# Performance work log

Hardware: AMD Instinct MI355X
Metric: run time of the kernel (lower is better)

## Reference

```python
import jax, jax.numpy as jnp
import numpy as np

N_NODES = 50000
N_EDGES = 800000
N_GRAPHS = 64
IN_CH = 128
GLOBAL_DIM = 256
HIDDEN = 64
HEADS = 4
N_CLASSES = 10


def setup_inputs() -> dict:
    key = jax.random.key(0)
    ks = jax.random.split(key, 32)
    lin = lambda k, fi, fo: jax.random.normal(k, (fi, fo), jnp.float32) * 0.02
    inp = {}
    inp["x"] = jax.random.normal(ks[0], (N_NODES, IN_CH), jnp.float32)
    inp["edge_index"] = jax.random.randint(ks[1], (2, N_EDGES), 0, N_NODES)
    inp["batch"] = jnp.sort(jax.random.randint(ks[2], (N_NODES,), 0, N_GRAPHS))
    inp["global_feats"] = jax.random.normal(ks[3], (N_GRAPHS, GLOBAL_DIM), jnp.float32)
    # conv1 (in=IN_CH)
    inp["c1_Wq"] = lin(ks[4], IN_CH, HEADS * HIDDEN); inp["c1_bq"] = jnp.zeros((HEADS * HIDDEN,), jnp.float32)
    inp["c1_Wk"] = lin(ks[5], IN_CH, HEADS * HIDDEN); inp["c1_bk"] = jnp.zeros((HEADS * HIDDEN,), jnp.float32)
    inp["c1_Wv"] = lin(ks[6], IN_CH, HEADS * HIDDEN); inp["c1_bv"] = jnp.zeros((HEADS * HIDDEN,), jnp.float32)
    inp["c1_Ws"] = lin(ks[7], IN_CH, HIDDEN);         inp["c1_bs"] = jnp.zeros((HIDDEN,), jnp.float32)
    # conv2 (in=HIDDEN)
    inp["c2_Wq"] = lin(ks[8], HIDDEN, HEADS * HIDDEN); inp["c2_bq"] = jnp.zeros((HEADS * HIDDEN,), jnp.float32)
    inp["c2_Wk"] = lin(ks[9], HIDDEN, HEADS * HIDDEN); inp["c2_bk"] = jnp.zeros((HEADS * HIDDEN,), jnp.float32)
    inp["c2_Wv"] = lin(ks[10], HIDDEN, HEADS * HIDDEN); inp["c2_bv"] = jnp.zeros((HEADS * HIDDEN,), jnp.float32)
    inp["c2_Ws"] = lin(ks[11], HIDDEN, HIDDEN);         inp["c2_bs"] = jnp.zeros((HIDDEN,), jnp.float32)
    # global MLP
    inp["g_W1"] = lin(ks[12], GLOBAL_DIM, HIDDEN); inp["g_b1"] = jnp.zeros((HIDDEN,), jnp.float32)
    inp["g_W2"] = lin(ks[13], HIDDEN, HIDDEN);     inp["g_b2"] = jnp.zeros((HIDDEN,), jnp.float32)
    # head
    inp["h_W1"] = lin(ks[14], 2 * HIDDEN, HIDDEN); inp["h_b1"] = jnp.zeros((HIDDEN,), jnp.float32)
    inp["h_W2"] = lin(ks[15], HIDDEN, N_CLASSES); inp["h_b2"] = jnp.zeros((N_CLASSES,), jnp.float32)
    return inp


def _tconv(x, src, dst, Wq, bq, Wk, bk, Wv, bv, Ws, bs):
    """PyG TransformerConv, heads=HEADS, concat=False (head-mean), root skip, eval-mode (no dropout)."""
    N = x.shape[0]
    q = (x @ Wq + bq).reshape(N, HEADS, HIDDEN)
    k = (x @ Wk + bk).reshape(N, HEADS, HIDDEN)
    v = (x @ Wv + bv).reshape(N, HEADS, HIDDEN)
    # per-edge attention logits  [E, H]
    s = jnp.einsum('ehd,ehd->eh', q[dst], k[src]) / jnp.sqrt(jnp.float32(HIDDEN))
    # segment softmax over incoming edges of each dst node
    m = jax.ops.segment_max(s, dst, num_segments=N)           # [N, H]
    e = jnp.exp(s - m[dst])                                    # [E, H]
    z = jax.ops.segment_sum(e, dst, num_segments=N)           # [N, H]
    alpha = e / z[dst]                                         # [E, H] (dst always has >=1 edge here)
    agg = jax.ops.segment_sum(alpha[:, :, None] * v[src], dst, num_segments=N)  # [N, H, D]
    return agg.mean(axis=1) + x @ Ws + bs


def reference(x, edge_index, batch, global_feats,
              c1_Wq, c1_bq, c1_Wk, c1_bk, c1_Wv, c1_bv, c1_Ws, c1_bs,
              c2_Wq, c2_bq, c2_Wk, c2_bk, c2_Wv, c2_bv, c2_Ws, c2_bs,
              g_W1, g_b1, g_W2, g_b2, h_W1, h_b1, h_W2, h_b2):
    src, dst = edge_index[0], edge_index[1]
    h = jax.nn.relu(_tconv(x, src, dst, c1_Wq, c1_bq, c1_Wk, c1_bk, c1_Wv, c1_bv, c1_Ws, c1_bs))
    h = jax.nn.relu(_tconv(h, src, dst, c2_Wq, c2_bq, c2_Wk, c2_bk, c2_Wv, c2_bv, c2_Ws, c2_bs))
    # global mean pool per graph
    ssum = jax.ops.segment_sum(h, batch, num_segments=N_GRAPHS)                # [G, HIDDEN]
    cnt = jax.ops.segment_sum(jnp.ones((h.shape[0],), h.dtype), batch, num_segments=N_GRAPHS)
    patch_emb = ssum / jnp.maximum(cnt, 1.0)[:, None]
    g = jax.nn.relu(global_feats @ g_W1 + g_b1)
    g = jax.nn.relu(g @ g_W2 + g_b2)
    fused = jnp.concatenate([patch_emb, g], axis=-1)
    return jax.nn.relu(fused @ h_W1 + h_b1) @ h_W2 + h_b2
```

## Files before the change

### kernel.cpp

```cpp
#include <hip/hip_runtime.h>
#include <hip/hip_bf16.h>
#include <math.h>

#define N_NODES   50000
#define N_EDGES   800000
#define N_GRAPHS  64
#define IN_CH     128
#define GLOBAL_DIM 256
#define HIDDEN    64
#define HEADS     4
#define N_CLASSES 10
#define QKV_COLS  832
#define MAXDEG    64

typedef unsigned short ushort_t;
typedef unsigned int uint_t;
typedef unsigned char uchar_t;
typedef __attribute__((ext_vector_type(8))) short short8;
typedef __attribute__((ext_vector_type(4))) float floatx4;
typedef __attribute__((ext_vector_type(2))) float floatx2;

__device__ __forceinline__ ushort_t bf16rne(float f) {
    uint_t b = __float_as_uint(f);
    b += 0x7fffu + ((b >> 16) & 1u);
    return (ushort_t)(b >> 16);
}
__device__ __forceinline__ float4 bf4_unpack(uint_t lo, uint_t hi) {
    float4 f;
    f.x = __uint_as_float(lo << 16);
    f.y = __uint_as_float(lo & 0xffff0000u);
    f.z = __uint_as_float(hi << 16);
    f.w = __uint_as_float(hi & 0xffff0000u);
    return f;
}
__device__ __forceinline__ uchar_t fp8e4m3(float f) {
    int v = __builtin_amdgcn_cvt_pk_fp8_f32(f, 0.f, 0, false);
    return (uchar_t)(v & 0xff);
}
__device__ __forceinline__ short8 pack_bf8(float4 a, float4 b) {
    union { short8 s; ushort_t u[8]; } r;
    r.u[0] = bf16rne(a.x); r.u[1] = bf16rne(a.y);
    r.u[2] = bf16rne(a.z); r.u[3] = bf16rne(a.w);
    r.u[4] = bf16rne(b.x); r.u[5] = bf16rne(b.y);
    r.u[6] = bf16rne(b.z); r.u[7] = bf16rne(b.w);
    return r.s;
}
__device__ __forceinline__ void graph_range(const int* __restrict__ batch, int g,
                                            int& start, int& end) {
    int lo = 0, hi = N_NODES;
    while (lo < hi) { int mid = (lo + hi) >> 1; if (batch[mid] < g) lo = mid + 1; else hi = mid; }
    start = lo;
    hi = N_NODES;
    while (lo < hi) { int mid = (lo + hi) >> 1; if (batch[mid] < g + 1) lo = mid + 1; else hi = mid; }
    end = lo;
}

#define PREP_CONC_B  624

__global__ __launch_bounds__(256) void prep2(
        const float* __restrict__ W1q, const float* __restrict__ W1k,
        const float* __restrict__ W1v, const float* __restrict__ W1s,
        const float* __restrict__ b1q, const float* __restrict__ b1k,
        const float* __restrict__ b1v, const float* __restrict__ b1s,
        const float* __restrict__ W2q, const float* __restrict__ W2k,
        const float* __restrict__ W2v, const float* __restrict__ W2s,
        const float* __restrict__ b2q, const float* __restrict__ b2k,
        const float* __restrict__ b2v, const float* __restrict__ b2s,
        ushort_t* __restrict__ Wt1, ushort_t* __restrict__ Wt2,
        float* __restrict__ bcat1, float* __restrict__ bcat2) {
    int idx = blockIdx.x * 256 + threadIdx.x;
    const int T1 = IN_CH * QKV_COLS;
    const int T2 = HIDDEN * QKV_COLS;
    if (idx < T1) {
        int c = idx / IN_CH, k = idx % IN_CH;
        float v;
        if (c < 256)      v = W1q[k * 256 + c];
        else if (c < 512) v = W1k[k * 256 + (c - 256)];
        else if (c < 768) v = W1v[k * 256 + (c - 512)];
        else              v = W1s[k * 64  + (c - 768)];
        Wt1[idx] = bf16rne(v);
    } else if (idx < T1 + T2) {
        int i2 = idx - T1;
        int c = i2 / HIDDEN, k = i2 % HIDDEN;
        float v;
        if (c < 256)      v = W2q[k * 256 + c];
        else if (c < 512) v = W2k[k * 256 + (c - 256)];
        else if (c < 768) v = W2v[k * 256 + (c - 512)];
        else              v = W2s[k * 64  + (c - 768)];
        Wt2[i2] = bf16rne(v);
    }
    if (idx < QKV_COLS) {
        float bb, b2;
        if (idx < 256)      { bb = b1q[idx];       b2 = b2q[idx]; }
        else if (idx < 512) { bb = b1k[idx - 256]; b2 = b2k[idx - 256]; }
        else if (idx < 768) { bb = b1v[idx - 512]; b2 = b2v[idx - 512]; }
        else                { bb = b1s[idx - 768]; b2 = b2s[idx - 768]; }
        bcat1[idx] = bb;
        bcat2[idx] = b2;
    }
}

template <int K, bool A_FP32>
__device__ __forceinline__ void gemm_body9(int idx0, int t,
                                           const void* __restrict__ Av,
                                           const ushort_t* __restrict__ Wt,
                                           const float* __restrict__ bias,
                                           uchar_t* __restrict__ qb8,
                                           uchar_t* __restrict__ kvb,
                                           ushort_t* __restrict__ skipb,
                                           int N, int RB, uchar_t* smem) {
    constexpr int KP = K + 8;
    constexpr int C8 = K / 8;
    ushort_t* Bs = (ushort_t*)smem;

    const int xcd = idx0 & 7;
    const int j = idx0 >> 3;
    const int ct = j % 13;
    const int strip = (j / 13) * 8 + xcd;
    if (strip >= RB) return;
    const int base_r = strip * 128;
    const int base_c = ct * 64;

#pragma unroll
    for (int i = 0; i < (64 * C8) / 256; ++i) {
        int ii = t + i * 256;
        int n = ii / C8, c = ii % C8;
        *(uint4*)(Bs + n * KP + c * 8) =
            *(const uint4*)(Wt + (size_t)(base_c + n) * K + c * 8);
    }

    const int wave = t >> 6, lane = t & 63;
    const int quad = lane >> 4, m16 = lane & 15;

    int arow0 = base_r + wave * 32 + m16;
    int arow1 = arow0 + 16;
    int cr0 = arow0 < N ? arow0 : N - 1;
    int cr1 = arow1 < N ? arow1 : N - 1;
    short8 a0[K / 32], a1[K / 32];
    if (A_FP32) {
        const float* A = (const float*)Av;
        const float* Ar0 = A + (size_t)cr0 * K + quad * 8;
        const float* Ar1 = A + (size_t)cr1 * K + quad * 8;
#pragma unroll
        for (int kc = 0; kc < K / 32; ++kc) {
            float4 f0 = *(const float4*)(Ar0 + kc * 32);
            float4 f1 = *(const float4*)(Ar0 + kc * 32 + 4);
            a0[kc] = pack_bf8(f0, f1);
            float4 g0 = *(const float4*)(Ar1 + kc * 32);
            float4 g1 = *(const float4*)(Ar1 + kc * 32 + 4);
            a1[kc] = pack_bf8(g0, g1);
        }
    } else {
        const ushort_t* A = (const ushort_t*)Av;
        const ushort_t* Ar0 = A + (size_t)cr0 * K + quad * 8;
        const ushort_t* Ar1 = A + (size_t)cr1 * K + quad * 8;
#pragma unroll
        for (int kc = 0; kc < K / 32; ++kc) {
            a0[kc] = *(const short8*)(Ar0 + kc * 32);
            a1[kc] = *(const short8*)(Ar1 + kc * 32);
        }
    }
    __syncthreads();

    floatx4 acc[2][4];
#pragma unroll
    for (int rt = 0; rt < 2; ++rt)
#pragma unroll
        for (int c2 = 0; c2 < 4; ++c2) acc[rt][c2] = (floatx4){0.f, 0.f, 0.f, 0.f};
#pragma unroll
    for (int kc = 0; kc < K / 32; ++kc) {
        int ko = kc * 32 + quad * 8;
#pragma unroll
        for (int c2 = 0; c2 < 4; ++c2) {
            short8 b = *(const short8*)(Bs + (c2 * 16 + m16) * KP + ko);
            acc[0][c2] = __builtin_amdgcn_mfma_f32_16x16x32_bf16(a0[kc], b, acc[0][c2], 0, 0, 0);
            acc[1][c2] = __builtin_amdgcn_mfma_f32_16x16x32_bf16(a1[kc], b, acc[1][c2], 0, 0, 0);
        }
    }

    float bb[4];
#pragma unroll
    for (int c2 = 0; c2 < 4; ++c2) bb[c2] = bias[base_c + c2 * 16 + m16];
#pragma unroll
    for (int rt = 0; rt < 2; ++rt)
#pragma unroll
        for (int c2 = 0; c2 < 4; ++c2)
#pragma unroll
            for (int r = 0; r < 4; ++r) acc[rt][c2][r] += bb[c2];

    __syncthreads();

    if (ct < 12) {
        uchar_t* ep = smem;
#pragma unroll
        for (int c2 = 0; c2 < 4; ++c2) {
            int col_l = c2 * 16 + m16;
#pragma unroll
            for (int rt = 0; rt < 2; ++rt)
#pragma unroll
                for (int r = 0; r < 4; ++r)
                    ep[(wave * 32 + rt * 16 + quad * 4 + r) * 80 + col_l] =
                        fp8e4m3(acc[rt][c2][r]);
        }
        __syncthreads();
        if (ct < 4) {
#pragma unroll
            for (int i = 0; i < 2; ++i) {
                int ii = t + i * 256;
                int row = ii >> 2, ch = ii & 3;
                int gr = base_r + row;
                if (gr < N)
                    *(uint4*)(qb8 + (size_t)gr * 256 + base_c + ch * 16) =
                        *(const uint4*)(ep + row * 80 + ch * 16);
            }
        } else {
            const bool isv = (ct >= 8);
            const int dim0base = isv ? (base_c - 512) : (base_c - 256);
            const int vo = isv ? 8 : 0;
#pragma unroll
            for (int i = 0; i < 2; ++i) {
                int ii = t + i * 256;
                int row = ii >> 2, ch = ii & 3;
                int gr = base_r + row;
                int cb = ((dim0base + ch * 16) << 1) + vo;
                if (gr < N) {
                    *(uint2*)(kvb + (size_t)gr * 512 + cb) =
                        *(const uint2*)(ep + row * 80 + ch * 16);
                    *(uint2*)(kvb + (size_t)gr * 512 + cb + 16) =
                        *(const uint2*)(ep + row * 80 + ch * 16 + 8);
                }
            }
        }
    } else {
        ushort_t* ep = (ushort_t*)smem;
#pragma unroll
        for (int c2 = 0; c2 < 4; ++c2) {
            int col_l = c2 * 16 + m16;
#pragma unroll
            for (int rt = 0; rt < 2; ++rt)
#pragma unroll
                for (int r = 0; r < 4; ++r)
                    ep[(wave * 32 + rt * 16 + quad * 4 + r) * 68 + col_l] =
                        bf16rne(acc[rt][c2][r]);
        }
        __syncthreads();
#pragma unroll
        for (int i = 0; i < 4; ++i) {
            int ii = t + i * 256;
            int row = ii >> 3, ch = ii & 7;
            int gr = base_r + row;
            if (gr < N)
                *(uint4*)(skipb + (size_t)gr * 64 + ch * 8) =
                    *(const uint4*)(ep + row * 68 + ch * 8);
        }
    }
}

#define FB2 782
template <int K, bool A_FP32>
__global__ __launch_bounds__(256) void gemm_fill9(const void* __restrict__ Av,
                                                  const ushort_t* __restrict__ Wt,
                                                  const float* __restrict__ bias,
                                                  uchar_t* __restrict__ qb8,
                                                  uchar_t* __restrict__ kvb,
                                                  ushort_t* __restrict__ skipb,
                                                  int N, int RB,
                                                  const int* __restrict__ src,
                                                  const int* __restrict__ dst,
                                                  int* __restrict__ cnt,
                                                  ushort_t* __restrict__ col) {
    __shared__ uchar_t smem[17408] __attribute__((aligned(16)));
    int t = threadIdx.x;
    int idx = (int)blockIdx.x;
    if (idx < FB2) {
        int e0 = idx * 1024 + t;
#pragma unroll
        for (int jj = 0; jj < 4; ++jj) {
            int e = e0 + jj * 256;
            if (e < N_EDGES) {
                int d = dst[e];
                int pos = atomicAdd(&cnt[d], 1);
                col[(d << 6) + pos] = (ushort_t)src[e];
            }
        }
        return;
    }
    gemm_body9<K, A_FP32>(idx - FB2, t, Av, Wt, bias, qb8, kvb, skipb, N, RB, smem);
}

template <int K, bool A_FP32>
__global__ __launch_bounds__(256) void gemm_v9(const void* __restrict__ Av,
                                               const ushort_t* __restrict__ Wt,
                                               const float* __restrict__ bias,
                                               uchar_t* __restrict__ qb8,
                                               uchar_t* __restrict__ kvb,
                                               ushort_t* __restrict__ skipb,
                                               int N, int RB) {
    __shared__ uchar_t smem[17408] __attribute__((aligned(16)));
    gemm_body9<K, A_FP32>((int)blockIdx.x, threadIdx.x, Av, Wt, bias,
                          qb8, kvb, skipb, N, RB, smem);
}

__device__ __forceinline__ void edge_step3(uint2 k8, uint2 v8, const floatx2* qp,
                                           float& z, floatx2* acp) {
    floatx2 dp = qp[0] * __builtin_amdgcn_cvt_pk_f32_fp8(k8.x, false);
    dp += qp[1] * __builtin_amdgcn_cvt_pk_f32_fp8(k8.x, true);
    dp += qp[2] * __builtin_amdgcn_cvt_pk_f32_fp8(k8.y, false);
    dp += qp[3] * __builtin_amdgcn_cvt_pk_f32_fp8(k8.y, true);
    float d = dp[0] + dp[1];
    d += __shfl_xor(d, 1);
    d += __shfl_xor(d, 2);
    d += __shfl_xor(d, 4);
    float p = __expf(d);
    z += p;
    floatx2 pp = {p, p};
    acp[0] += pp * __builtin_amdgcn_cvt_pk_f32_fp8(v8.x, false);
    acp[1] += pp * __builtin_amdgcn_cvt_pk_f32_fp8(v8.x, true);
    acp[2] += pp * __builtin_amdgcn_cvt_pk_f32_fp8(v8.y, false);
    acp[3] += pp * __builtin_amdgcn_cvt_pk_f32_fp8(v8.y, true);
}

template <bool OUT_BF16>
__global__ __launch_bounds__(256) void attn_agg7(const uchar_t* __restrict__ qb8,
                                                 const uchar_t* __restrict__ kvb,
                                                 const ushort_t* __restrict__ skipb,
                                                 const int* __restrict__ deg,
                                                 const ushort_t* __restrict__ col,
                                                 void* __restrict__ hout) {
    int node = blockIdx.x * 4 + threadIdx.y;
    if (node >= N_NODES) return;
    int lane = threadIdx.x;
    int half = lane >> 5, sl = lane & 31;
    uint2 qd = *(const uint2*)(qb8 + (size_t)node * 256 + sl * 8);
    const floatx2 s8 = {0.125f, 0.125f};
    floatx2 qp[4];
    qp[0] = s8 * __builtin_amdgcn_cvt_pk_f32_fp8(qd.x, false);
    qp[1] = s8 * __builtin_amdgcn_cvt_pk_f32_fp8(qd.x, true);
    qp[2] = s8 * __builtin_amdgcn_cvt_pk_f32_fp8(qd.y, false);
    qp[3] = s8 * __builtin_amdgcn_cvt_pk_f32_fp8(qd.y, true);
    floatx2 acp[4];
    acp[0] = (floatx2){0.f, 0.f}; acp[1] = (floatx2){0.f, 0.f};
    acp[2] = (floatx2){0.f, 0.f}; acp[3] = (floatx2){0.f, 0.f};
    float z = 0.f;
    int dv = deg[node];
    int creg = (int)col[(node << 6) | lane];
    int e = half;
    const uchar_t* kb = kvb + (size_t)sl * 16;
    for (; e + 6 < dv; e += 8) {
        int c0 = __shfl(creg, e);
        int c1 = __shfl(creg, e + 2);
        int c2 = __shfl(creg, e + 4);
        int c3 = __shfl(creg, e + 6);
        uint4 x0 = *(const uint4*)(kb + (size_t)c0 * 512);
        uint4 x1 = *(const uint4*)(kb + (size_t)c1 * 512);
        uint4 x2 = *(const uint4*)(kb + (size_t)c2 * 512);
        uint4 x3 = *(const uint4*)(kb + (size_t)c3 * 512);
        edge_step3(make_uint2(x0.x, x0.y), make_uint2(x0.z, x0.w), qp, z, acp);
        edge_step3(make_uint2(x1.x, x1.y), make_uint2(x1.z, x1.w), qp, z, acp);
        edge_step3(make_uint2(x2.x, x2.y), make_uint2(x2.z, x2.w), qp, z, acp);
        edge_step3(make_uint2(x3.x, x3.y), make_uint2(x3.z, x3.w), qp, z, acp);
    }
    for (; e < dv; e += 2) {
        int c0 = __shfl(creg, e);
        uint4 x0 = *(const uint4*)(kb + (size_t)c0 * 512);
        edge_step3(make_uint2(x0.x, x0.y), make_uint2(x0.z, x0.w), qp, z, acp);
    }
    z += __shfl_xor(z, 32);
    float ac[8] = {acp[0][0], acp[0][1], acp[1][0], acp[1][1],
                   acp[2][0], acp[2][1], acp[3][0], acp[3][1]};
#pragma unroll
    for (int i = 0; i < 8; ++i) ac[i] += __shfl_xor(ac[i], 32);
    float inv = (z > 0.f) ? (0.25f / z) : 0.f;
#pragma unroll
    for (int i = 0; i < 8; ++i) ac[i] *= inv;
#pragma unroll
    for (int i = 0; i < 8; ++i) {
        ac[i] += __shfl_xor(ac[i], 8);
        ac[i] += __shfl_xor(ac[i], 16);
    }
    if (lane < 8) {
        uint4 su = *(const uint4*)(skipb + (size_t)node * 64 + lane * 8);
        float4 s0 = bf4_unpack(su.x, su.y);
        float4 s1 = bf4_unpack(su.z, su.w);
        float o0 = fmaxf(ac[0] + s0.x, 0.f);
        float o1 = fmaxf(ac[1] + s0.y, 0.f);
        float o2 = fmaxf(ac[2] + s0.z, 0.f);
        float o3 = fmaxf(ac[3] + s0.w, 0.f);
        float o4 = fmaxf(ac[4] + s1.x, 0.f);
        float o5 = fmaxf(ac[5] + s1.y, 0.f);
        float o6 = fmaxf(ac[6] + s1.z, 0.f);
        float o7 = fmaxf(ac[7] + s1.w, 0.f);
        if (OUT_BF16) {
            uint4 u;
            u.x = (uint_t)bf16rne(o0) | ((uint_t)bf16rne(o1) << 16);
            u.y = (uint_t)bf16rne(o2) | ((uint_t)bf16rne(o3) << 16);
            u.z = (uint_t)bf16rne(o4) | ((uint_t)bf16rne(o5) << 16);
            u.w = (uint_t)bf16rne(o6) | ((uint_t)bf16rne(o7) << 16);
            *(uint4*)((ushort_t*)hout + (size_t)node * HIDDEN + lane * 8) = u;
        } else {
            float* op = (float*)hout + (size_t)node * HIDDEN + lane * 8;
            *(float4*)(op)     = make_float4(o0, o1, o2, o3);
            *(float4*)(op + 4) = make_float4(o4, o5, o6, o7);
        }
    }
}

__global__ __launch_bounds__(256) void pool_partial(const float* __restrict__ h,
                                                    const int* __restrict__ batch,
                                                    float* __restrict__ part) {
    int g = blockIdx.x >> 3;
    int s = blockIdx.x & 7;
    int start, end;
    graph_range(batch, g, start, end);
    int len = end - start;
    int s0 = start + (len * s) / 8;
    int s1 = start + (len * (s + 1)) / 8;
    int t = threadIdx.x;
    int d = t & 63, chunk = t >> 6;
    float acc = 0.f;
    for (int n = s0 + chunk; n < s1; n += 4) acc += h[(size_t)n * HIDDEN + d];
    __shared__ float sh[256];
    sh[t] = acc;
    __syncthreads();
    if (t < 64)
        part[(size_t)blockIdx.x * 64 + t] = sh[t] + sh[64 + t] + sh[128 + t] + sh[192 + t];
}

__global__ __launch_bounds__(256) void head_mlp(const float* __restrict__ part,
                                                const int* __restrict__ batch,
                                                const float* __restrict__ gf,
                                                const float* __restrict__ gW1, const float* __restrict__ gb1,
                                                const float* __restrict__ gW2, const float* __restrict__ gb2,
                                                const float* __restrict__ hW1, const float* __restrict__ hb1,
                                                const float* __restrict__ hW2, const float* __restrict__ hb2,
                                                float* __restrict__ out) {
    int g = blockIdx.x;
    int t = threadIdx.x;
    int d = t & 63, kk = t >> 6;
    int start, end;
    graph_range(batch, g, start, end);
    float cnt = fmaxf((float)(end - start), 1.0f);
    __shared__ float gfs[GLOBAL_DIM];
    __shared__ float fused[2 * HIDDEN];
    __shared__ float g1[HIDDEN];
    __shared__ float h1s[HIDDEN];
    __shared__ float red[256];
    gfs[t] = gf[(size_t)g * GLOBAL_DIM + t];
    if (t < 64) {
        float s = 0.f;
#pragma unroll
        for (int i = 0; i < 8; ++i) s += part[((size_t)g * 8 + i) * 64 + t];
        fused[t] = s / cnt;
    }
    __syncthreads();
    {
        float a = 0.f;
        int k0 = kk * 64;
#pragma unroll 4
        for (int k = k0; k < k0 + 64; ++k) a = fmaf(gfs[k], gW1[k * HIDDEN + d], a);
        red[t] = a;
        __syncthreads();
        if (t < 64) g1[t] = fmaxf(red[t] + red[64 + t] + red[128 + t] + red[192 + t] + gb1[t], 0.f);
        __syncthreads();
    }
    {
        float a = 0.f;
        int k0 = kk * 16;
#pragma unroll 4
        for (int k = k0; k < k0 + 16; ++k) a = fmaf(g1[k], gW2[k * HIDDEN + d], a);
        red[t] = a;
        __syncthreads();
        if (t < 64) fused[HIDDEN + t] =
            fmaxf(red[t] + red[64 + t] + red[128 + t] + red[192 + t] + gb2[t], 0.f);
        __syncthreads();
    }
    {
        float a = 0.f;
        int k0 = kk * 32;
#pragma unroll 4
        for (int k = k0; k < k0 + 32; ++k) a = fmaf(fused[k], hW1[k * HIDDEN + d], a);
        red[t] = a;
        __syncthreads();
        if (t < 64) h1s[t] = fmaxf(red[t] + red[64 + t] + red[128 + t] + red[192 + t] + hb1[t], 0.f);
        __syncthreads();
    }
    if (t < N_CLASSES) {
        float o = hb2[t];
#pragma unroll 4
        for (int k = 0; k < HIDDEN; ++k) o = fmaf(h1s[k], hW2[k * N_CLASSES + t], o);
        out[(size_t)g * N_CLASSES + t] = o;
    }
}

extern "C" void kernel_launch(void* const* d_in, const int* in_sizes, int n_in,
                              void* d_out, int out_size, void* d_ws, size_t ws_size,
                              hipStream_t stream) {
    const float* x        = (const float*)d_in[0];
    const int*   eidx     = (const int*)d_in[1];
    const int*   batch    = (const int*)d_in[2];
    const float* gfeats   = (const float*)d_in[3];
    const float* c1_Wq = (const float*)d_in[4];  const float* c1_bq = (const float*)d_in[5];
    const float* c1_Wk = (const float*)d_in[6];  const float* c1_bk = (const float*)d_in[7];
    const float* c1_Wv = (const float*)d_in[8];  const float* c1_bv = (const float*)d_in[9];
    const float* c1_Ws = (const float*)d_in[10]; const float* c1_bs = (const float*)d_in[11];
    const float* c2_Wq = (const float*)d_in[12]; const float* c2_bq = (const float*)d_in[13];
    const float* c2_Wk = (const float*)d_in[14]; const float* c2_bk = (const float*)d_in[15];
    const float* c2_Wv = (const float*)d_in[16]; const float* c2_bv = (const float*)d_in[17];
    const float* c2_Ws = (const float*)d_in[18]; const float* c2_bs = (const float*)d_in[19];
    const float* g_W1 = (const float*)d_in[20]; const float* g_b1 = (const float*)d_in[21];
    const float* g_W2 = (const float*)d_in[22]; const float* g_b2 = (const float*)d_in[23];
    const float* h_W1 = (const float*)d_in[24]; const float* h_b1 = (const float*)d_in[25];
    const float* h_W2 = (const float*)d_in[26]; const float* h_b2 = (const float*)d_in[27];
    float* out = (float*)d_out;

    const int* srcp = eidx;
    const int* dstp = eidx + N_EDGES;

    char* base = (char*)d_ws;
    uchar_t*  kvb  = (uchar_t*)base;  base += (size_t)N_NODES * 512;
    uchar_t*  qb8  = (uchar_t*)base;  base += (size_t)N_NODES * 256;
    ushort_t* skipb = (ushort_t*)base; base += (size_t)N_NODES * HIDDEN * 2;
    ushort_t* h1b  = (ushort_t*)base; base += (size_t)N_NODES * HIDDEN * 2;
    float*    h2   = (float*)base;    base += (size_t)N_NODES * HIDDEN * 4;
    ushort_t* Wt1  = (ushort_t*)base; base += (size_t)IN_CH * QKV_COLS * 2;
    ushort_t* Wt2  = (ushort_t*)base; base += (size_t)HIDDEN * QKV_COLS * 2;
    float*    bcat1 = (float*)base;   base += QKV_COLS * 4;
    float*    bcat2 = (float*)base;   base += QKV_COLS * 4;
    float*    part = (float*)base;    base += (size_t)N_GRAPHS * 8 * 64 * 4;
    int*      deg  = (int*)base;      base += (size_t)N_NODES * 4;
    ushort_t* colb = (ushort_t*)base; base += ((size_t)N_NODES * MAXDEG + 64) * 2;

    const int RB = (N_NODES + 127) / 128;
    const int GG = 8 * 13 * ((RB + 7) / 8);
    dim3 attn_block(64, 4);
    int attn_grid = (N_NODES + 3) / 4;

    hipMemsetAsync(deg, 0, N_NODES * sizeof(int), stream);
    prep2<<<PREP_CONC_B, 256, 0, stream>>>(
        c1_Wq, c1_Wk, c1_Wv, c1_Ws, c1_bq, c1_bk, c1_bv, c1_bs,
        c2_Wq, c2_Wk, c2_Wv, c2_Ws, c2_bq, c2_bk, c2_bv, c2_bs,
        Wt1, Wt2, bcat1, bcat2);

    gemm_fill9<IN_CH, true><<<FB2 + GG, 256, 0, stream>>>(
        x, Wt1, bcat1, qb8, kvb, skipb, N_NODES, RB, srcp, dstp, deg, colb);
    attn_agg7<true><<<attn_grid, attn_block, 0, stream>>>(qb8, kvb, skipb, deg, colb, h1b);

    gemm_v9<HIDDEN, false><<<GG, 256, 0, stream>>>(h1b, Wt2, bcat2, qb8, kvb, skipb, N_NODES, RB);
    attn_agg7<false><<<attn_grid, attn_block, 0, stream>>>(qb8, kvb, skipb, deg, colb, h2);

    pool_partial<<<N_GRAPHS * 8, 256, 0, stream>>>(h2, batch, part);
    head_mlp<<<N_GRAPHS, 256, 0, stream>>>(part, batch, gfeats,
                                           g_W1, g_b1, g_W2, g_b2,
                                           h_W1, h_b1, h_W2, h_b2, out);
}
```

Measured before the change: 386.8 us.

## Build CSR adjacency via two-pass bucketed binning with shared-memory atomics

Edge-to-CSR construction becomes two passes. In the first pass, extra blocks appended to the weight-prep kernel bin edges by destination bucket (256 nodes each) into per-block slabs. In the second pass, one block per bucket scatters the edges into the column array using shared-memory atomic counters, then writes out the degrees. This replaces one global atomic per edge and removes the separate memset of the degree array. The cost is a larger intermediate slab, stored in the not-yet-used h2 buffer, and a per-slab cap of 80 entries that would silently drop edges if a bucket overflows.

```diff
diff --git a/kernel.cpp b/kernel.cpp
--- a/kernel.cpp
+++ b/kernel.cpp
@@ -13,6 +13,11 @@
 #define QKV_COLS  832
 #define MAXDEG    64
 
+#define P1B    128
+#define EPB    6250
+#define NBUCK  196
+#define SLABP  80
+
 typedef unsigned short ushort_t;
 typedef unsigned int uint_t;
 typedef unsigned char uchar_t;
@@ -57,7 +62,7 @@
 
 #define PREP_CONC_B  624
 
-__global__ __launch_bounds__(256) void prep2(
+__global__ __launch_bounds__(256) void prep_p1(
         const float* __restrict__ W1q, const float* __restrict__ W1k,
         const float* __restrict__ W1v, const float* __restrict__ W1s,
         const float* __restrict__ b1q, const float* __restrict__ b1k,
@@ -67,8 +72,31 @@
         const float* __restrict__ b2q, const float* __restrict__ b2k,
         const float* __restrict__ b2v, const float* __restrict__ b2s,
         ushort_t* __restrict__ Wt1, ushort_t* __restrict__ Wt2,
-        float* __restrict__ bcat1, float* __restrict__ bcat2) {
-    int idx = blockIdx.x * 256 + threadIdx.x;
+        float* __restrict__ bcat1, float* __restrict__ bcat2,
+        const int* __restrict__ src, const int* __restrict__ dst,
+        uint_t* __restrict__ slab, int* __restrict__ cntm) {
+    int b = blockIdx.x, t = threadIdx.x;
+    if (b >= PREP_CONC_B) {
+        int blk = b - PREP_CONC_B;
+        __shared__ int hist[NBUCK];
+        for (int i = t; i < NBUCK; i += 256) hist[i] = 0;
+        __syncthreads();
+        int e0 = blk * EPB;
+        int e1 = e0 + EPB;
+        for (int e = e0 + t; e < e1; e += 256) {
+            int s = src[e], d = dst[e];
+            int bu = d >> 8;
+            int off = atomicAdd(&hist[bu], 1);
+            if (off < SLABP)
+                slab[((size_t)bu * P1B + blk) * SLABP + off] =
+                    ((uint_t)d << 16) | (uint_t)s;
+        }
+        __syncthreads();
+        for (int i = t; i < NBUCK; i += 256)
+            cntm[i * P1B + blk] = hist[i] < SLABP ? hist[i] : SLABP;
+        return;
+    }
+    int idx = b * 256 + t;
     const int T1 = IN_CH * QKV_COLS;
     const int T2 = HIDDEN * QKV_COLS;
     if (idx < T1) {
@@ -256,7 +284,6 @@
     }
 }
 
-#define FB2 782
 template <int K, bool A_FP32>
 __global__ __launch_bounds__(256) void gemm_fill9(const void* __restrict__ Av,
                                                   const ushort_t* __restrict__ Wt,
@@ -265,27 +292,36 @@
                                                   uchar_t* __restrict__ kvb,
                                                   ushort_t* __restrict__ skipb,
                                                   int N, int RB,
-                                                  const int* __restrict__ src,
-                                                  const int* __restrict__ dst,
-                                                  int* __restrict__ cnt,
+                                                  const int* __restrict__ cntm,
+                                                  const uint_t* __restrict__ slab,
+                                                  int* __restrict__ deg,
                                                   ushort_t* __restrict__ col) {
     __shared__ uchar_t smem[17408] __attribute__((aligned(16)));
     int t = threadIdx.x;
     int idx = (int)blockIdx.x;
-    if (idx < FB2) {
-        int e0 = idx * 1024 + t;
-#pragma unroll
-        for (int jj = 0; jj < 4; ++jj) {
-            int e = e0 + jj * 256;
-            if (e < N_EDGES) {
-                int d = dst[e];
-                int pos = atomicAdd(&cnt[d], 1);
-                col[(d << 6) + pos] = (ushort_t)src[e];
+    if (idx < NBUCK) {
+        __shared__ int cnt2[256];
+        __shared__ int cs[P1B];
+        if (t < P1B) cs[t] = cntm[idx * P1B + t];
+        cnt2[t] = 0;
+        __syncthreads();
+        const uint_t* myslab = slab + (size_t)idx * P1B * SLABP;
+        for (int i = t; i < P1B * SLABP; i += 256) {
+            int blkq = i / SLABP;
+            int off = i - blkq * SLABP;
+            if (off < cs[blkq]) {
+                uint_t rec = myslab[i];
+                int d = rec >> 16;
+                int pos = atomicAdd(&cnt2[d & 255], 1);
+                col[((size_t)d << 6) + pos] = (ushort_t)(rec & 0xffffu);
             }
         }
+        __syncthreads();
+        int gn = (idx << 8) + t;
+        if (gn < N_NODES) deg[gn] = cnt2[t];
         return;
     }
-    gemm_body9<K, A_FP32>(idx - FB2, t, Av, Wt, bias, qb8, kvb, skipb, N, RB, smem);
+    gemm_body9<K, A_FP32>(idx - NBUCK, t, Av, Wt, bias, qb8, kvb, skipb, N, RB, smem);
 }
 
 template <int K, bool A_FP32>
@@ -530,19 +566,21 @@
     int*      deg  = (int*)base;      base += (size_t)N_NODES * 4;
     ushort_t* colb = (ushort_t*)base; base += ((size_t)N_NODES * MAXDEG + 64) * 2;
 
+    uint_t* slab = (uint_t*)h2;
+    int*    cntm = (int*)((char*)h2 + (size_t)NBUCK * P1B * SLABP * 4);
+
     const int RB = (N_NODES + 127) / 128;
     const int GG = 8 * 13 * ((RB + 7) / 8);
     dim3 attn_block(64, 4);
     int attn_grid = (N_NODES + 3) / 4;
 
-    hipMemsetAsync(deg, 0, N_NODES * sizeof(int), stream);
-    prep2<<<PREP_CONC_B, 256, 0, stream>>>(
+    prep_p1<<<PREP_CONC_B + P1B, 256, 0, stream>>>(
         c1_Wq, c1_Wk, c1_Wv, c1_Ws, c1_bq, c1_bk, c1_bv, c1_bs,
         c2_Wq, c2_Wk, c2_Wv, c2_Ws, c2_bq, c2_bk, c2_bv, c2_bs,
-        Wt1, Wt2, bcat1, bcat2);
-
-    gemm_fill9<IN_CH, true><<<FB2 + GG, 256, 0, stream>>>(
-        x, Wt1, bcat1, qb8, kvb, skipb, N_NODES, RB, srcp, dstp, deg, colb);
+        Wt1, Wt2, bcat1, bcat2, srcp, dstp, slab, cntm);
+
+    gemm_fill9<IN_CH, true><<<NBUCK + GG, 256, 0, stream>>>(
+        x, Wt1, bcat1, qb8, kvb, skipb, N_NODES, RB, cntm, slab, deg, colb);
     attn_agg7<true><<<attn_grid, attn_block, 0, stream>>>(qb8, kvb, skipb, deg, colb, h1b);
 
     gemm_v9<HIDDEN, false><<<GG, 256, 0, stream>>>(h1b, Wt2, bcat2, qb8, kvb, skipb, N_NODES, RB);
```

Measured after the change: 353.2 us. 1.09x faster.
